# Performance work log

Hardware: AMD Instinct MI355X
Metric: run time of the kernel (lower is better)

## Reference

```python
import jax, jax.numpy as jnp
import numpy as np

N_NODES = 100000
N_EDGES = 3200000
D_IN = 128
UNITS = 128


def setup_inputs() -> dict:
    key = jax.random.key(0)
    k1, k2, k3, k4, k5, k6 = jax.random.split(key, 6)
    x = jax.random.normal(k1, (N_NODES, D_IN), dtype=jnp.float32)
    edge_src = jax.random.randint(k2, (N_EDGES,), 0, N_NODES, dtype=jnp.int32)
    edge_dst = jax.random.randint(k3, (N_EDGES,), 0, N_NODES, dtype=jnp.int32)
    edge_vals = jax.random.uniform(k4, (N_EDGES,), dtype=jnp.float32)
    w = jax.random.normal(k5, (D_IN, UNITS), dtype=jnp.float32) * (2.0 / D_IN) ** 0.5  # he_normal scale
    b = jax.random.normal(k6, (UNITS,), dtype=jnp.float32) * 0.05
    return {"x": x, "edge_src": edge_src, "edge_dst": edge_dst,
            "edge_vals": edge_vals, "w": w, "b": b}


def reference(x, edge_src, edge_dst, edge_vals, w, b):
    # dense transform: [N, D_IN] @ [D_IN, UNITS] -> [N, UNITS]
    h = x @ w
    # sparse adjacency SpMM via edge list: out[dst] += val * h[src]
    msgs = edge_vals[:, None] * h[edge_src]  # [E, UNITS]
    agg = jax.ops.segment_sum(msgs, edge_dst, num_segments=N_NODES)
    # fused bias + relu epilogue
    return jax.nn.relu(agg + b)
```

## Files before the change

### kernel.cpp

```cpp
#include <hip/hip_runtime.h>

#define NODES 100000
#define EDGES 3200000
#define D 128
#define NBUCKET ((NODES + 255) / 256)
#define NBUCKP 392
#define CH 4096
#define NB_BIN ((EDGES + CH - 1) / CH)
#define CAP 10240

typedef unsigned short us8 __attribute__((ext_vector_type(8)));
typedef _Float16 half8 __attribute__((ext_vector_type(8)));
typedef _Float16 h2 __attribute__((ext_vector_type(2)));
typedef float f32x4 __attribute__((ext_vector_type(4)));

__device__ __forceinline__ unsigned short f32_to_f16_bits(float f) {
    return __builtin_bit_cast(unsigned short, (_Float16)f);
}
__device__ __forceinline__ h2 uh2(unsigned u) {
    return __builtin_bit_cast(h2, u);
}

__global__ __launch_bounds__(256) void wprep(const float* __restrict__ w,
                                             unsigned short* __restrict__ wt) {
    int i = blockIdx.x * 256 + threadIdx.x;
    if (i >= 16384) return;
    int j  = i & 7;
    int l  = (i >> 3) & 63;
    int c  = (i >> 9) & 3;
    int ct = i >> 11;
    int k   = 32 * c + ((l >> 4) << 3) + j;
    int col = (ct << 4) + (l & 15);
    wt[i] = f32_to_f16_bits(w[k * D + col]);
}

__global__ __launch_bounds__(256) void gemm_mfma(const float* __restrict__ x,
                                                 const unsigned short* __restrict__ wt,
                                                 unsigned short* __restrict__ hb) {
    __shared__ unsigned short wl[16384];
    const int tid = threadIdx.x;
    for (int i = tid; i < 2048; i += 256)
        ((us8*)wl)[i] = ((const us8*)wt)[i];
    __syncthreads();

    const int wave = tid >> 6, lane = tid & 63;
    const long r0 = ((long)blockIdx.x * 4 + wave) * 16;
    if (r0 >= NODES) return;
    const int m = lane & 15, q = lane >> 4;
    const float* xr = x + (r0 + m) * D;

    f32x4 acc[8];
#pragma unroll
    for (int ct = 0; ct < 8; ct++) acc[ct] = (f32x4){0.f, 0.f, 0.f, 0.f};

#pragma unroll
    for (int c = 0; c < 4; c++) {
        const int k0 = 32 * c + 8 * q;
        float4 xa = *(const float4*)(xr + k0);
        float4 xb = *(const float4*)(xr + k0 + 4);
        half8 a;
        a[0] = (_Float16)xa.x;
        a[1] = (_Float16)xa.y;
        a[2] = (_Float16)xa.z;
        a[3] = (_Float16)xa.w;
        a[4] = (_Float16)xb.x;
        a[5] = (_Float16)xb.y;
        a[6] = (_Float16)xb.z;
        a[7] = (_Float16)xb.w;
#pragma unroll
        for (int ct = 0; ct < 8; ct++) {
            half8 bfr = *(const half8*)&wl[(((ct << 2) + c) * 64 + lane) * 8];
            acc[ct] = __builtin_amdgcn_mfma_f32_16x16x32_f16(a, bfr, acc[ct], 0, 0, 0);
        }
    }

#pragma unroll
    for (int ct = 0; ct < 8; ct++) {
#pragma unroll
        for (int r = 0; r < 4; r++) {
            int row = q * 4 + r;
            hb[(r0 + row) * D + ct * 16 + m] = f32_to_f16_bits(acc[ct][r]);
        }
    }
}

__global__ __launch_bounds__(512) void bin_pass1(const int* __restrict__ esrc,
                                                 const int* __restrict__ edst,
                                                 const float* __restrict__ eval,
                                                 int* __restrict__ bcur,
                                                 int2* __restrict__ tmp) {
    __shared__ int2 sed[CH];
    __shared__ int hist[NBUCKP];
    __shared__ int basel[NBUCKP];
    __shared__ int lcur[NBUCKP];
    __shared__ int gbase[NBUCKP];
    __shared__ int wsum[8];
    const int tid = threadIdx.x;
    const long e0 = (long)blockIdx.x * CH;
    const int n = (int)((EDGES - e0 < CH) ? (EDGES - e0) : CH);

    for (int bk = tid; bk < NBUCKP; bk += 512) { hist[bk] = 0; lcur[bk] = 0; }
    __syncthreads();

    unsigned pk[8];
    int ds[8];
#pragma unroll
    for (int u = 0; u < 8; u++) {
        int i = tid + u * 512;
        if (i < n) {
            long e = e0 + i;
            int dst = edst[e];
            unsigned hv = (unsigned)f32_to_f16_bits(eval[e]);
            pk[u] = (hv << 17) | (unsigned)esrc[e];
            ds[u] = dst;
            atomicAdd(&hist[dst >> 8], 1);
        } else {
            ds[u] = -1;
        }
    }
    __syncthreads();

    int h0 = 0, h1 = 0;
    if (tid < 196) { h0 = hist[2 * tid]; h1 = hist[2 * tid + 1]; }
    int s = h0 + h1;
    int lane = tid & 63, wid = tid >> 6;
    int sc = s;
#pragma unroll
    for (int off = 1; off < 64; off <<= 1) {
        int t = __shfl_up(sc, off, 64);
        if (lane >= off) sc += t;
    }
    if (lane == 63) wsum[wid] = sc;
    __syncthreads();
    int wb = 0;
    for (int w2 = 0; w2 < wid && w2 < 4; w2++) wb += wsum[w2];
    int excl = wb + sc - s;
    if (tid < 196) { basel[2 * tid] = excl; basel[2 * tid + 1] = excl + h0; }
    for (int bk = tid; bk < NBUCKET; bk += 512) {
        int c = hist[bk];
        if (c > 0) gbase[bk] = bk * CAP + atomicAdd(&bcur[bk], c);
    }
    __syncthreads();

#pragma unroll
    for (int u = 0; u < 8; u++) {
        if (ds[u] >= 0) {
            int bk = ds[u] >> 8;
            int lp = basel[bk] + atomicAdd(&lcur[bk], 1);
            sed[lp] = make_int2((int)pk[u], ds[u]);
        }
    }
    __syncthreads();

    for (int i = tid; i < n; i += 512) {
        int2 t = sed[i];
        int bk = t.y >> 8;
        tmp[gbase[bk] + (i - basel[bk])] = t;
    }
}

__global__ __launch_bounds__(512) void bin_pass2(const int* __restrict__ bcur,
                                                 const int2* __restrict__ tmp,
                                                 int* __restrict__ rpd,
                                                 unsigned* __restrict__ epk) {
    __shared__ unsigned spk[CAP];
    __shared__ unsigned char sd8[CAP];
    __shared__ int cnt[256];
    __shared__ int pos[256];
    __shared__ int wsum[4];
    const int b = blockIdx.x;
    const int tid = threadIdx.x;
    const int beg = b * CAP;
    const int n = bcur[b];

    for (int i = tid; i < 256; i += 512) cnt[i] = 0;
    __syncthreads();
    for (int i = tid; i < n; i += 512) {
        int2 t = tmp[beg + i];
        spk[i] = (unsigned)t.x;
        int d8 = t.y & 255;
        sd8[i] = (unsigned char)d8;
        atomicAdd(&cnt[d8], 1);
    }
    __syncthreads();

    if (tid < 256) {
        int v = cnt[tid];
        int lane = tid & 63, wid = tid >> 6;
        int s = v;
#pragma unroll
        for (int off = 1; off < 64; off <<= 1) {
            int t = __shfl_up(s, off, 64);
            if (lane >= off) s += t;
        }
        if (lane == 63) wsum[wid] = s;
        __syncthreads();
        int wbase = 0;
        for (int w = 0; w < wid; w++) wbase += wsum[w];
        int excl = wbase + s - v;
        pos[tid] = excl;
        int node = (b << 8) + tid;
        if (node < NODES) rpd[node] = (((beg << 1) + excl) << 8) | v;
    } else {
        __syncthreads();
    }
    __syncthreads();

    for (int i = tid; i < n; i += 512) {
        int p = atomicAdd(&pos[sd8[i]], 1);
        epk[(beg << 1) + p] = spk[i];
    }
}

__global__ __launch_bounds__(256) void aggregate(const int* __restrict__ rpd,
                                                 const unsigned* __restrict__ epack,
                                                 const unsigned short* __restrict__ hb,
                                                 const float* __restrict__ bias,
                                                 float* __restrict__ out) {
    const int lane = threadIdx.x & 63;
    const int node = blockIdx.x * 4 + (threadIdx.x >> 6);
    if (node >= NODES) return;
    const int sub = lane >> 4;
    const int li  = lane & 15;
    const int v = rpd[node];
    const int beg = (int)(((unsigned)v) >> 8);
    const int end = beg + (v & 255);
    const unsigned short* hp = hb + li * 8;

    h2 aA0 = (h2)0, aA1 = (h2)0, aA2 = (h2)0, aA3 = (h2)0;
    h2 aB0 = (h2)0, aB1 = (h2)0, aB2 = (h2)0, aB3 = (h2)0;

    for (int e0 = beg + sub; e0 < end; e0 += 16) {
        int i0 = e0, i1 = e0 + 4, i2 = e0 + 8, i3 = e0 + 12;
        unsigned p0 = epack[i0];
        unsigned p1 = (i1 < end) ? epack[i1] : 0u;
        unsigned p2 = (i2 < end) ? epack[i2] : 0u;
        unsigned p3 = (i3 < end) ? epack[i3] : 0u;

        unsigned s0 = p0 & 0x1FFFFu, s1 = p1 & 0x1FFFFu;
        unsigned s2 = p2 & 0x1FFFFu, s3 = p3 & 0x1FFFFu;
        unsigned v0 = p0 >> 17, v1 = p1 >> 17, v2 = p2 >> 17, v3 = p3 >> 17;

        uint4 r0 = *(const uint4*)(hp + (size_t)s0 * D);
        uint4 r1 = *(const uint4*)(hp + (size_t)s1 * D);
        uint4 r2 = *(const uint4*)(hp + (size_t)s2 * D);
        uint4 r3 = *(const uint4*)(hp + (size_t)s3 * D);

        h2 w0 = uh2(v0 | (v0 << 16));
        h2 w1 = uh2(v1 | (v1 << 16));
        h2 w2 = uh2(v2 | (v2 << 16));
        h2 w3 = uh2(v3 | (v3 << 16));

        aA0 = uh2(r0.x) * w0 + aA0;
        aA1 = uh2(r0.y) * w0 + aA1;
        aA2 = uh2(r0.z) * w0 + aA2;
        aA3 = uh2(r0.w) * w0 + aA3;
        aB0 = uh2(r1.x) * w1 + aB0;
        aB1 = uh2(r1.y) * w1 + aB1;
        aB2 = uh2(r1.z) * w1 + aB2;
        aB3 = uh2(r1.w) * w1 + aB3;
        aA0 = uh2(r2.x) * w2 + aA0;
        aA1 = uh2(r2.y) * w2 + aA1;
        aA2 = uh2(r2.z) * w2 + aA2;
        aA3 = uh2(r2.w) * w2 + aA3;
        aB0 = uh2(r3.x) * w3 + aB0;
        aB1 = uh2(r3.y) * w3 + aB1;
        aB2 = uh2(r3.z) * w3 + aB2;
        aB3 = uh2(r3.w) * w3 + aB3;
    }

    h2 m0 = aA0 + aB0, m1 = aA1 + aB1, m2 = aA2 + aB2, m3 = aA3 + aB3;
    float r[8];
    r[0] = (float)m0[0]; r[1] = (float)m0[1];
    r[2] = (float)m1[0]; r[3] = (float)m1[1];
    r[4] = (float)m2[0]; r[5] = (float)m2[1];
    r[6] = (float)m3[0]; r[7] = (float)m3[1];
#pragma unroll
    for (int k = 0; k < 8; k++) {
        r[k] += __shfl_xor(r[k], 16, 64);
        r[k] += __shfl_xor(r[k], 32, 64);
    }

    if (sub == 0) {
        const float* bp = bias + li * 8;
        float4 b0 = *(const float4*)bp;
        float4 b1 = *(const float4*)(bp + 4);
        float4 o0, o1;
        o0.x = fmaxf(r[0] + b0.x, 0.f);
        o0.y = fmaxf(r[1] + b0.y, 0.f);
        o0.z = fmaxf(r[2] + b0.z, 0.f);
        o0.w = fmaxf(r[3] + b0.w, 0.f);
        o1.x = fmaxf(r[4] + b1.x, 0.f);
        o1.y = fmaxf(r[5] + b1.y, 0.f);
        o1.z = fmaxf(r[6] + b1.z, 0.f);
        o1.w = fmaxf(r[7] + b1.w, 0.f);
        float* op = out + (size_t)node * D + li * 8;
        *(float4*)op = o0;
        *(float4*)(op + 4) = o1;
    }
}

extern "C" void kernel_launch(void* const* d_in, const int* in_sizes, int n_in,
                              void* d_out, int out_size, void* d_ws, size_t ws_size,
                              hipStream_t stream) {
    const float* x    = (const float*)d_in[0];
    const int*   esrc = (const int*)  d_in[1];
    const int*   edst = (const int*)  d_in[2];
    const float* eval = (const float*)d_in[3];
    const float* w    = (const float*)d_in[4];
    const float* b    = (const float*)d_in[5];
    float* out = (float*)d_out;

    char* ws = (char*)d_ws;
    const size_t OFF_H    = 0;
    const size_t OFF_WT   = 25600000;
    const size_t OFF_RPD  = OFF_WT   + 32768;
    const size_t OFF_BCUR = OFF_RPD  + 400128;
    const size_t OFF_TMP  = OFF_BCUR + 2048;

    unsigned short* hb   = (unsigned short*)(ws + OFF_H);
    unsigned short* wt   = (unsigned short*)(ws + OFF_WT);
    int*            rpd  = (int*)           (ws + OFF_RPD);
    int*            bcur = (int*)           (ws + OFF_BCUR);
    int2*           tmp  = (int2*)          (ws + OFF_TMP);
    unsigned*       epk  = (unsigned*)      (ws + OFF_TMP);

    hipMemsetAsync(bcur, 0, NBUCKET * sizeof(int), stream);
    wprep<<<64, 256, 0, stream>>>(w, wt);
    gemm_mfma<<<(NODES + 63) / 64, 256, 0, stream>>>(x, wt, hb);
    bin_pass1<<<NB_BIN, 512, 0, stream>>>(esrc, edst, eval, bcur, tmp);
    bin_pass2<<<NBUCKET, 512, 0, stream>>>(bcur, tmp, rpd, epk);
    aggregate<<<(NODES + 3) / 4, 256, 0, stream>>>(rpd, epk, hb, b, out);
}
```

Before: 293.4 us.

## Fuse per-bucket counting sort with aggregation and rebucket nodes into 196-node bins

Merges the second binning pass and the aggregation kernel into one kernel. Each of 512 blocks sorts its bucket's edges by destination into shared memory, then aggregates the bucket's 196 nodes directly from that shared list. Buckets now hold 196 nodes each (computed with a magic-number division) so there are exactly 512 buckets, one per block. This removes the global write and read of the sorted edge array and the row-pointer array, plus one launch. The cost is far less parallelism in aggregation (512 blocks of 8 waves, each wave walking many nodes) and a smaller per-bucket capacity, which could overflow on skewed inputs.

```diff
diff --git a/kernel.cpp b/kernel.cpp
--- a/kernel.cpp
+++ b/kernel.cpp
@@ -3,11 +3,12 @@
 #define NODES 100000
 #define EDGES 3200000
 #define D 128
-#define NBUCKET ((NODES + 255) / 256)
-#define NBUCKP 392
+#define NPB 196
+#define NB2 512
 #define CH 4096
 #define NB_BIN ((EDGES + CH - 1) / CH)
-#define CAP 10240
+#define CAP 7168
+#define MAGIC196 175304788u
 
 typedef unsigned short us8 __attribute__((ext_vector_type(8)));
 typedef _Float16 half8 __attribute__((ext_vector_type(8)));
@@ -19,6 +20,9 @@
 }
 __device__ __forceinline__ h2 uh2(unsigned u) {
     return __builtin_bit_cast(h2, u);
+}
+__device__ __forceinline__ int div196(int dst) {
+    return (int)(__umulhi((unsigned)dst, MAGIC196) >> 3);
 }
 
 __global__ __launch_bounds__(256) void wprep(const float* __restrict__ w,
@@ -90,16 +94,16 @@
                                                  int* __restrict__ bcur,
                                                  int2* __restrict__ tmp) {
     __shared__ int2 sed[CH];
-    __shared__ int hist[NBUCKP];
-    __shared__ int basel[NBUCKP];
-    __shared__ int lcur[NBUCKP];
-    __shared__ int gbase[NBUCKP];
+    __shared__ int hist[NB2];
+    __shared__ int basel[NB2];
+    __shared__ int lcur[NB2];
+    __shared__ int gbase[NB2];
     __shared__ int wsum[8];
     const int tid = threadIdx.x;
     const long e0 = (long)blockIdx.x * CH;
     const int n = (int)((EDGES - e0 < CH) ? (EDGES - e0) : CH);
 
-    for (int bk = tid; bk < NBUCKP; bk += 512) { hist[bk] = 0; lcur[bk] = 0; }
+    for (int bk = tid; bk < NB2; bk += 512) { hist[bk] = 0; lcur[bk] = 0; }
     __syncthreads();
 
     unsigned pk[8];
@@ -110,10 +114,12 @@
         if (i < n) {
             long e = e0 + i;
             int dst = edst[e];
+            int bk = div196(dst);
+            int d8 = dst - bk * NPB;
             unsigned hv = (unsigned)f32_to_f16_bits(eval[e]);
             pk[u] = (hv << 17) | (unsigned)esrc[e];
-            ds[u] = dst;
-            atomicAdd(&hist[dst >> 8], 1);
+            ds[u] = (bk << 8) | d8;
+            atomicAdd(&hist[bk], 1);
         } else {
             ds[u] = -1;
         }
@@ -121,7 +127,7 @@
     __syncthreads();
 
     int h0 = 0, h1 = 0;
-    if (tid < 196) { h0 = hist[2 * tid]; h1 = hist[2 * tid + 1]; }
+    if (tid < 256) { h0 = hist[2 * tid]; h1 = hist[2 * tid + 1]; }
     int s = h0 + h1;
     int lane = tid & 63, wid = tid >> 6;
     int sc = s;
@@ -135,8 +141,8 @@
     int wb = 0;
     for (int w2 = 0; w2 < wid && w2 < 4; w2++) wb += wsum[w2];
     int excl = wb + sc - s;
-    if (tid < 196) { basel[2 * tid] = excl; basel[2 * tid + 1] = excl + h0; }
-    for (int bk = tid; bk < NBUCKET; bk += 512) {
+    if (tid < 256) { basel[2 * tid] = excl; basel[2 * tid + 1] = excl + h0; }
+    for (int bk = tid; bk < NB2; bk += 512) {
         int c = hist[bk];
         if (c > 0) gbase[bk] = bk * CAP + atomicAdd(&bcur[bk], c);
     }
@@ -159,144 +165,136 @@
     }
 }
 
-__global__ __launch_bounds__(512) void bin_pass2(const int* __restrict__ bcur,
-                                                 const int2* __restrict__ tmp,
-                                                 int* __restrict__ rpd,
-                                                 unsigned* __restrict__ epk) {
+__global__ __launch_bounds__(512) void sort_agg(const int* __restrict__ bcur,
+                                                const int2* __restrict__ tmp,
+                                                const unsigned short* __restrict__ hb,
+                                                const float* __restrict__ bias,
+                                                float* __restrict__ out) {
     __shared__ unsigned spk[CAP];
-    __shared__ unsigned char sd8[CAP];
     __shared__ int cnt[256];
-    __shared__ int pos[256];
+    __shared__ int pos[257];
+    __shared__ int cur[256];
     __shared__ int wsum[4];
+    const int tid = threadIdx.x;
     const int b = blockIdx.x;
-    const int tid = threadIdx.x;
-    const int beg = b * CAP;
     const int n = bcur[b];
-
-    for (int i = tid; i < 256; i += 512) cnt[i] = 0;
-    __syncthreads();
-    for (int i = tid; i < n; i += 512) {
-        int2 t = tmp[beg + i];
-        spk[i] = (unsigned)t.x;
-        int d8 = t.y & 255;
-        sd8[i] = (unsigned char)d8;
-        atomicAdd(&cnt[d8], 1);
-    }
-    __syncthreads();
-
+    const long base = (long)b * CAP;
+    const int lane = tid & 63, wid = tid >> 6;
+
+    if (tid < 256) cnt[tid] = 0;
+    __syncthreads();
+    for (int i = tid; i < n; i += 512)
+        atomicAdd(&cnt[tmp[base + i].y & 255], 1);
+    __syncthreads();
+
+    int v = 0, s = 0;
     if (tid < 256) {
-        int v = cnt[tid];
-        int lane = tid & 63, wid = tid >> 6;
-        int s = v;
+        v = cnt[tid];
+        s = v;
 #pragma unroll
         for (int off = 1; off < 64; off <<= 1) {
             int t = __shfl_up(s, off, 64);
             if (lane >= off) s += t;
         }
         if (lane == 63) wsum[wid] = s;
-        __syncthreads();
-        int wbase = 0;
-        for (int w = 0; w < wid; w++) wbase += wsum[w];
-        int excl = wbase + s - v;
+    }
+    __syncthreads();
+    if (tid < 256) {
+        int wb = 0;
+        for (int w2 = 0; w2 < wid; w2++) wb += wsum[w2];
+        int excl = wb + s - v;
         pos[tid] = excl;
-        int node = (b << 8) + tid;
-        if (node < NODES) rpd[node] = (((beg << 1) + excl) << 8) | v;
-    } else {
-        __syncthreads();
+        cur[tid] = excl;
+        if (tid == 255) pos[256] = excl + v;
     }
     __syncthreads();
 
     for (int i = tid; i < n; i += 512) {
-        int p = atomicAdd(&pos[sd8[i]], 1);
-        epk[(beg << 1) + p] = spk[i];
-    }
-}
-
-__global__ __launch_bounds__(256) void aggregate(const int* __restrict__ rpd,
-                                                 const unsigned* __restrict__ epack,
-                                                 const unsigned short* __restrict__ hb,
-                                                 const float* __restrict__ bias,
-                                                 float* __restrict__ out) {
-    const int lane = threadIdx.x & 63;
-    const int node = blockIdx.x * 4 + (threadIdx.x >> 6);
-    if (node >= NODES) return;
-    const int sub = lane >> 4;
-    const int li  = lane & 15;
-    const int v = rpd[node];
-    const int beg = (int)(((unsigned)v) >> 8);
-    const int end = beg + (v & 255);
+        int2 t = tmp[base + i];
+        int p = atomicAdd(&cur[t.y & 255], 1);
+        spk[p] = (unsigned)t.x;
+    }
+    __syncthreads();
+
+    const int sub = lane >> 4, li = lane & 15;
     const unsigned short* hp = hb + li * 8;
-
-    h2 aA0 = (h2)0, aA1 = (h2)0, aA2 = (h2)0, aA3 = (h2)0;
-    h2 aB0 = (h2)0, aB1 = (h2)0, aB2 = (h2)0, aB3 = (h2)0;
-
-    for (int e0 = beg + sub; e0 < end; e0 += 16) {
-        int i0 = e0, i1 = e0 + 4, i2 = e0 + 8, i3 = e0 + 12;
-        unsigned p0 = epack[i0];
-        unsigned p1 = (i1 < end) ? epack[i1] : 0u;
-        unsigned p2 = (i2 < end) ? epack[i2] : 0u;
-        unsigned p3 = (i3 < end) ? epack[i3] : 0u;
-
-        unsigned s0 = p0 & 0x1FFFFu, s1 = p1 & 0x1FFFFu;
-        unsigned s2 = p2 & 0x1FFFFu, s3 = p3 & 0x1FFFFu;
-        unsigned v0 = p0 >> 17, v1 = p1 >> 17, v2 = p2 >> 17, v3 = p3 >> 17;
-
-        uint4 r0 = *(const uint4*)(hp + (size_t)s0 * D);
-        uint4 r1 = *(const uint4*)(hp + (size_t)s1 * D);
-        uint4 r2 = *(const uint4*)(hp + (size_t)s2 * D);
-        uint4 r3 = *(const uint4*)(hp + (size_t)s3 * D);
-
-        h2 w0 = uh2(v0 | (v0 << 16));
-        h2 w1 = uh2(v1 | (v1 << 16));
-        h2 w2 = uh2(v2 | (v2 << 16));
-        h2 w3 = uh2(v3 | (v3 << 16));
-
-        aA0 = uh2(r0.x) * w0 + aA0;
-        aA1 = uh2(r0.y) * w0 + aA1;
-        aA2 = uh2(r0.z) * w0 + aA2;
-        aA3 = uh2(r0.w) * w0 + aA3;
-        aB0 = uh2(r1.x) * w1 + aB0;
-        aB1 = uh2(r1.y) * w1 + aB1;
-        aB2 = uh2(r1.z) * w1 + aB2;
-        aB3 = uh2(r1.w) * w1 + aB3;
-        aA0 = uh2(r2.x) * w2 + aA0;
-        aA1 = uh2(r2.y) * w2 + aA1;
-        aA2 = uh2(r2.z) * w2 + aA2;
-        aA3 = uh2(r2.w) * w2 + aA3;
-        aB0 = uh2(r3.x) * w3 + aB0;
-        aB1 = uh2(r3.y) * w3 + aB1;
-        aB2 = uh2(r3.z) * w3 + aB2;
-        aB3 = uh2(r3.w) * w3 + aB3;
-    }
-
-    h2 m0 = aA0 + aB0, m1 = aA1 + aB1, m2 = aA2 + aB2, m3 = aA3 + aB3;
-    float r[8];
-    r[0] = (float)m0[0]; r[1] = (float)m0[1];
-    r[2] = (float)m1[0]; r[3] = (float)m1[1];
-    r[4] = (float)m2[0]; r[5] = (float)m2[1];
-    r[6] = (float)m3[0]; r[7] = (float)m3[1];
-#pragma unroll
-    for (int k = 0; k < 8; k++) {
-        r[k] += __shfl_xor(r[k], 16, 64);
-        r[k] += __shfl_xor(r[k], 32, 64);
-    }
-
-    if (sub == 0) {
-        const float* bp = bias + li * 8;
-        float4 b0 = *(const float4*)bp;
-        float4 b1 = *(const float4*)(bp + 4);
-        float4 o0, o1;
-        o0.x = fmaxf(r[0] + b0.x, 0.f);
-        o0.y = fmaxf(r[1] + b0.y, 0.f);
-        o0.z = fmaxf(r[2] + b0.z, 0.f);
-        o0.w = fmaxf(r[3] + b0.w, 0.f);
-        o1.x = fmaxf(r[4] + b1.x, 0.f);
-        o1.y = fmaxf(r[5] + b1.y, 0.f);
-        o1.z = fmaxf(r[6] + b1.z, 0.f);
-        o1.w = fmaxf(r[7] + b1.w, 0.f);
-        float* op = out + (size_t)node * D + li * 8;
-        *(float4*)op = o0;
-        *(float4*)(op + 4) = o1;
+    const float* bp = bias + li * 8;
+    const float4 b0 = *(const float4*)bp;
+    const float4 b1 = *(const float4*)(bp + 4);
+
+    for (int nd = wid; nd < NPB; nd += 8) {
+        int node = b * NPB + nd;
+        if (node >= NODES) break;
+        const int beg = pos[nd], end = pos[nd + 1];
+
+        h2 aA0 = (h2)0, aA1 = (h2)0, aA2 = (h2)0, aA3 = (h2)0;
+        h2 aB0 = (h2)0, aB1 = (h2)0, aB2 = (h2)0, aB3 = (h2)0;
+
+        for (int e0 = beg + sub; e0 < end; e0 += 16) {
+            int i0 = e0, i1 = e0 + 4, i2 = e0 + 8, i3 = e0 + 12;
+            unsigned p0 = spk[i0];
+            unsigned p1 = (i1 < end) ? spk[i1] : 0u;
+            unsigned p2 = (i2 < end) ? spk[i2] : 0u;
+            unsigned p3 = (i3 < end) ? spk[i3] : 0u;
+
+            unsigned s0 = p0 & 0x1FFFFu, s1 = p1 & 0x1FFFFu;
+            unsigned s2 = p2 & 0x1FFFFu, s3 = p3 & 0x1FFFFu;
+            unsigned v0 = p0 >> 17, v1 = p1 >> 17, v2 = p2 >> 17, v3 = p3 >> 17;
+
+            uint4 r0 = *(const uint4*)(hp + (size_t)s0 * D);
+            uint4 r1 = *(const uint4*)(hp + (size_t)s1 * D);
+            uint4 r2 = *(const uint4*)(hp + (size_t)s2 * D);
+            uint4 r3 = *(const uint4*)(hp + (size_t)s3 * D);
+
+            h2 w0 = uh2(v0 | (v0 << 16));
+            h2 w1 = uh2(v1 | (v1 << 16));
+            h2 w2 = uh2(v2 | (v2 << 16));
+            h2 w3 = uh2(v3 | (v3 << 16));
+
+            aA0 = uh2(r0.x) * w0 + aA0;
+            aA1 = uh2(r0.y) * w0 + aA1;
+            aA2 = uh2(r0.z) * w0 + aA2;
+            aA3 = uh2(r0.w) * w0 + aA3;
+            aB0 = uh2(r1.x) * w1 + aB0;
+            aB1 = uh2(r1.y) * w1 + aB1;
+            aB2 = uh2(r1.z) * w1 + aB2;
+            aB3 = uh2(r1.w) * w1 + aB3;
+            aA0 = uh2(r2.x) * w2 + aA0;
+            aA1 = uh2(r2.y) * w2 + aA1;
+            aA2 = uh2(r2.z) * w2 + aA2;
+            aA3 = uh2(r2.w) * w2 + aA3;
+            aB0 = uh2(r3.x) * w3 + aB0;
+            aB1 = uh2(r3.y) * w3 + aB1;
+            aB2 = uh2(r3.z) * w3 + aB2;
+            aB3 = uh2(r3.w) * w3 + aB3;
+        }
+
+        h2 m0 = aA0 + aB0, m1 = aA1 + aB1, m2 = aA2 + aB2, m3 = aA3 + aB3;
+        float r[8];
+        r[0] = (float)m0[0]; r[1] = (float)m0[1];
+        r[2] = (float)m1[0]; r[3] = (float)m1[1];
+        r[4] = (float)m2[0]; r[5] = (float)m2[1];
+        r[6] = (float)m3[0]; r[7] = (float)m3[1];
+#pragma unroll
+        for (int k = 0; k < 8; k++) {
+            r[k] += __shfl_xor(r[k], 16, 64);
+            r[k] += __shfl_xor(r[k], 32, 64);
+        }
+
+        if (sub == 0) {
+            float4 o0, o1;
+            o0.x = fmaxf(r[0] + b0.x, 0.f);
+            o0.y = fmaxf(r[1] + b0.y, 0.f);
+            o0.z = fmaxf(r[2] + b0.z, 0.f);
+            o0.w = fmaxf(r[3] + b0.w, 0.f);
+            o1.x = fmaxf(r[4] + b1.x, 0.f);
+            o1.y = fmaxf(r[5] + b1.y, 0.f);
+            o1.z = fmaxf(r[6] + b1.z, 0.f);
+            o1.w = fmaxf(r[7] + b1.w, 0.f);
+            float* op = out + (size_t)node * D + li * 8;
+            *(float4*)op = o0;
+            *(float4*)(op + 4) = o1;
+        }
     }
 }
 
@@ -314,21 +312,17 @@
     char* ws = (char*)d_ws;
     const size_t OFF_H    = 0;
     const size_t OFF_WT   = 25600000;
-    const size_t OFF_RPD  = OFF_WT   + 32768;
-    const size_t OFF_BCUR = OFF_RPD  + 400128;
+    const size_t OFF_BCUR = OFF_WT   + 32768;
     const size_t OFF_TMP  = OFF_BCUR + 2048;
 
     unsigned short* hb   = (unsigned short*)(ws + OFF_H);
     unsigned short* wt   = (unsigned short*)(ws + OFF_WT);
-    int*            rpd  = (int*)           (ws + OFF_RPD);
     int*            bcur = (int*)           (ws + OFF_BCUR);
     int2*           tmp  = (int2*)          (ws + OFF_TMP);
-    unsigned*       epk  = (unsigned*)      (ws + OFF_TMP);
-
-    hipMemsetAsync(bcur, 0, NBUCKET * sizeof(int), stream);
+
+    hipMemsetAsync(bcur, 0, NB2 * sizeof(int), stream);
     wprep<<<64, 256, 0, stream>>>(w, wt);
     gemm_mfma<<<(NODES + 63) / 64, 256, 0, stream>>>(x, wt, hb);
     bin_pass1<<<NB_BIN, 512, 0, stream>>>(esrc, edst, eval, bcur, tmp);
-    bin_pass2<<<NBUCKET, 512, 0, stream>>>(bcur, tmp, rpd, epk);
-    aggregate<<<(NODES + 3) / 4, 256, 0, stream>>>(rpd, epk, hb, b, out);
-}
+    sort_agg<<<NB2, 512, 0, stream>>>(bcur, tmp, hb, b, out);
+}
```

After: 286.0 us. 1.03x faster.
